# Kernel optimization log

Measured on AMD Instinct MI355X. Metric: run time of the kernel, lower is better.

The kernel has to match this reference:

```python
import jax, jax.numpy as jnp
import numpy as np

SEQ_LEN, INPUT_DIM, HIDDEN_DIM, OUTPUT_DIM = 512, 512, 1024, 512
BATCH = 64


def setup_inputs() -> dict:
    key = jax.random.key(0)
    k1, k2, k3, k4, k5 = jax.random.split(key, 5)
    fan_in_i2h = INPUT_DIM + HIDDEN_DIM
    s1 = 1.0 / np.sqrt(fan_in_i2h)
    s2 = 1.0 / np.sqrt(HIDDEN_DIM)
    return {
        "x": jax.random.normal(k1, (BATCH, SEQ_LEN, INPUT_DIM), dtype=jnp.float32),
        # i2h: Linear(input_dim+hidden_dim, 4*hidden_dim); stored as (in, out) for x @ W
        "W_i2h": jax.random.uniform(k2, (fan_in_i2h, 4 * HIDDEN_DIM), minval=-s1, maxval=s1, dtype=jnp.float32),
        "b_i2h": jax.random.uniform(k3, (4 * HIDDEN_DIM,), minval=-s1, maxval=s1, dtype=jnp.float32),
        # h2o: Linear(hidden_dim, output_dim)
        "W_h2o": jax.random.uniform(k4, (HIDDEN_DIM, OUTPUT_DIM), minval=-s2, maxval=s2, dtype=jnp.float32),
        "b_h2o": jax.random.uniform(k5, (OUTPUT_DIM,), minval=-s2, maxval=s2, dtype=jnp.float32),
    }


def reference(x, W_i2h, b_i2h, W_h2o, b_h2o):
    B = x.shape[0]
    H = W_h2o.shape[0]
    h0 = jnp.zeros((B, H), dtype=x.dtype)
    c0 = jnp.zeros((B, H), dtype=x.dtype)

    def step(carry, x_t):
        h_t, c_t = carry
        combined = jnp.concatenate([x_t, h_t], axis=1)  # [B, in+H]
        gates = combined @ W_i2h + b_i2h                # [B, 4H]
        i_t, f_t, g_t, o_t = jnp.split(gates, 4, axis=1)
        i_t = jax.nn.sigmoid(i_t)
        f_t = jax.nn.sigmoid(f_t)
        g_t = jnp.tanh(g_t)
        o_t = jax.nn.sigmoid(o_t)
        c_new = f_t * c_t + i_t * g_t
        h_new = o_t * jnp.tanh(c_new)
        return (h_new, c_new), None

    # scan over time: x [B, T, in] -> [T, B, in]
    (h_last, _), _ = jax.lax.scan(step, (h0, c0), jnp.swapaxes(x, 0, 1))
    # original returns only the last timestep's output projection
    return h_last @ W_h2o + b_h2o
```

## Files before the change

kernel.cpp:

```cpp
#include <hip/hip_runtime.h>
#include <hip/hip_bf16.h>
#include <stdint.h>


typedef __bf16 bf16x8 __attribute__((ext_vector_type(8)));
typedef float  f32x4  __attribute__((ext_vector_type(4)));
typedef unsigned long long u64;

#define NWG   256
#define NTHR  512

#define WS_FLAGS  0
#define WS_GO     2048
#define WS_HBUF   4096
#define HB_STRIDE 262144
#define HB_LO     131072
#define WS_HLAST  (WS_HBUF + 2*HB_STRIDE)

#define L_WHI   0
#define L_WLO   49152
#define L_EXCH  98304
#define L_EXCH2 102400
#define LDS_BYTES 106496

__device__ __forceinline__ float sigm(float x) {
    return __builtin_amdgcn_rcpf(1.0f + __expf(-x));
}
__device__ __forceinline__ float tanh_f(float x) {
    x = fminf(fmaxf(x, -20.0f), 20.0f);
    float e = __expf(-2.0f * x);
    return (1.0f - e) * __builtin_amdgcn_rcpf(1.0f + e);
}

__global__ void lstm_init(char* __restrict__ ws) {
    int id = blockIdx.x * 256 + threadIdx.x;
    for (int i = id; i < 66560; i += 256 * 256)
        __hip_atomic_store((unsigned*)ws + i, 0u,
                           __ATOMIC_RELAXED, __HIP_MEMORY_SCOPE_AGENT);
}

__global__ __launch_bounds__(NTHR) void lstm_main(
        const float* __restrict__ x, const float* __restrict__ Wi2h,
        const float* __restrict__ bi2h, const float* __restrict__ Wh2o,
        const float* __restrict__ bh2o, float* __restrict__ out,
        char* __restrict__ ws) {
    extern __shared__ char lds[];
    const int tid = threadIdx.x, wg = blockIdx.x;
    const int w = tid >> 6, lane = tid & 63, g = lane >> 4, nl = lane & 15;
    const int mt = w & 3, kh = w >> 2;

    for (int u = tid; u < 3072; u += NTHR) {
        int ak = u >> 4, cl = u & 15;
        int n = (cl >> 2) * 1024 + wg * 4 + (cl & 3);
        bf16x8 hi8, lo8;
#pragma unroll
        for (int j = 0; j < 8; ++j) {
            float v = Wi2h[(size_t)(ak * 8 + j) * 4096 + n];
            __bf16 h = (__bf16)v;
            hi8[j] = h;
            lo8[j] = (__bf16)(v - (float)h);
        }
        *(bf16x8*)(lds + L_WHI + (size_t)u * 16) = hi8;
        *(bf16x8*)(lds + L_WLO + (size_t)u * 16) = lo8;
    }
    const float bias_nl = bi2h[(nl >> 2) * 1024 + wg * 4 + (nl & 3)];
    __syncthreads();

    unsigned* flags = (unsigned*)(ws + WS_FLAGS);
    unsigned* go    = (unsigned*)(ws + WS_GO);
    float* exch  = (float*)(lds + L_EXCH);
    float* exch2 = (float*)(lds + L_EXCH2);
    float creg = 0.f;

#pragma unroll 1
    for (int t = 0; t < 512; ++t) {
        const char* hb_rd = ws + WS_HBUF + (size_t)(t & 1) * HB_STRIDE;
        char*       hb_wr = ws + WS_HBUF + (size_t)((t + 1) & 1) * HB_STRIDE;
        f32x4 acc0 = {0.f, 0.f, 0.f, 0.f}, acc1 = {0.f, 0.f, 0.f, 0.f};

        {
            const float* xb = x + ((size_t)(mt * 16 + nl) * 512 + t) * 512 + g * 8;
            const int s0 = kh * 8;
#pragma unroll
            for (int si = 0; si < 8; ++si) {
                const int s = s0 + si;
                float4 v0 = *(const float4*)(xb + s * 32);
                float4 v1 = *(const float4*)(xb + s * 32 + 4);
                float vv[8] = {v0.x, v0.y, v0.z, v0.w, v1.x, v1.y, v1.z, v1.w};
                bf16x8 ahi, alo;
#pragma unroll
                for (int j = 0; j < 8; ++j) {
                    __bf16 h = (__bf16)vv[j];
                    ahi[j] = h;
                    alo[j] = (__bf16)(vv[j] - (float)h);
                }
                const char* bp = lds + (size_t)(4 * s + g) * 256 + nl * 16;
                bf16x8 bhi = *(const bf16x8*)(bp + L_WHI);
                bf16x8 blo = *(const bf16x8*)(bp + L_WLO);
                if (s & 1) {
                    acc1 = __builtin_amdgcn_mfma_f32_16x16x32_bf16(ahi, bhi, acc1, 0, 0, 0);
                    acc1 = __builtin_amdgcn_mfma_f32_16x16x32_bf16(ahi, blo, acc1, 0, 0, 0);
                    acc1 = __builtin_amdgcn_mfma_f32_16x16x32_bf16(alo, bhi, acc1, 0, 0, 0);
                } else {
                    acc0 = __builtin_amdgcn_mfma_f32_16x16x32_bf16(ahi, bhi, acc0, 0, 0, 0);
                    acc0 = __builtin_amdgcn_mfma_f32_16x16x32_bf16(ahi, blo, acc0, 0, 0, 0);
                    acc0 = __builtin_amdgcn_mfma_f32_16x16x32_bf16(alo, bhi, acc0, 0, 0, 0);
                }
            }
        }

        if (tid == 0) {
            while (__hip_atomic_load(go, __ATOMIC_RELAXED,
                                     __HIP_MEMORY_SCOPE_AGENT) < (unsigned)t)
                __builtin_amdgcn_s_sleep(1);
        }
        __syncthreads();

        {
            const int s0 = 16 + kh * 16;
#pragma unroll 4
            for (int si = 0; si < 16; ++si) {
                const int s = s0 + si;
                size_t ha = ((size_t)(mt * 32 + (s - 16)) * 64 + lane) * 16;
                const char* bse = hb_rd + ha;
                u64 q0 = __hip_atomic_load((const u64*)(bse),
                           __ATOMIC_RELAXED, __HIP_MEMORY_SCOPE_AGENT);
                u64 q1 = __hip_atomic_load((const u64*)(bse + 8),
                           __ATOMIC_RELAXED, __HIP_MEMORY_SCOPE_AGENT);
                u64 q2 = __hip_atomic_load((const u64*)(bse + HB_LO),
                           __ATOMIC_RELAXED, __HIP_MEMORY_SCOPE_AGENT);
                u64 q3 = __hip_atomic_load((const u64*)(bse + HB_LO + 8),
                           __ATOMIC_RELAXED, __HIP_MEMORY_SCOPE_AGENT);
                union { u64 q[2]; bf16x8 v; } uh, ul;
                uh.q[0] = q0; uh.q[1] = q1;
                ul.q[0] = q2; ul.q[1] = q3;
                bf16x8 ahi = uh.v, alo = ul.v;
                const char* bp = lds + (size_t)(4 * s + g) * 256 + nl * 16;
                bf16x8 bhi = *(const bf16x8*)(bp + L_WHI);
                bf16x8 blo = *(const bf16x8*)(bp + L_WLO);
                if (s & 1) {
                    acc1 = __builtin_amdgcn_mfma_f32_16x16x32_bf16(ahi, bhi, acc1, 0, 0, 0);
                    acc1 = __builtin_amdgcn_mfma_f32_16x16x32_bf16(ahi, blo, acc1, 0, 0, 0);
                    acc1 = __builtin_amdgcn_mfma_f32_16x16x32_bf16(alo, bhi, acc1, 0, 0, 0);
                } else {
                    acc0 = __builtin_amdgcn_mfma_f32_16x16x32_bf16(ahi, bhi, acc0, 0, 0, 0);
                    acc0 = __builtin_amdgcn_mfma_f32_16x16x32_bf16(ahi, blo, acc0, 0, 0, 0);
                    acc0 = __builtin_amdgcn_mfma_f32_16x16x32_bf16(alo, bhi, acc0, 0, 0, 0);
                }
            }
        }

        if (kh == 1) {
#pragma unroll
            for (int j = 0; j < 4; ++j)
                exch[mt * 256 + (g * 4 + j) * 16 + nl] = acc0[j] + acc1[j];
        }
        __syncthreads();
        if (kh == 0) {
#pragma unroll
            for (int j = 0; j < 4; ++j) {
                float pre = acc0[j] + acc1[j] + exch[mt * 256 + (g * 4 + j) * 16 + nl]
                          + bias_nl;
                float act = ((nl >> 2) == 2) ? tanh_f(pre) : sigm(pre);
                exch2[mt * 256 + (g * 4 + j) * 16 + nl] = act;
            }
        }
        __syncthreads();
        if (tid < 256) {
            int mt2 = tid >> 6, r = (tid >> 2) & 15, hc = tid & 3;
            const float* a2 = exch2 + mt2 * 256 + r * 16;
            float iv = a2[hc], fv = a2[4 + hc], gv = a2[8 + hc], ov = a2[12 + hc];
            float cc = fv * creg + iv * gv;
            creg = cc;
            float hv = ov * tanh_f(cc);
            __bf16 hh = (__bf16)hv;
            __bf16 hl = (__bf16)(hv - (float)hh);
            int k = 512 + wg * 4 + hc;
            int hs = (k >> 5) - 16, kg = (k >> 3) & 3, j8 = k & 7;
            uint32_t ad = ((uint32_t)(mt2 * 32 + hs) * 64 + kg * 16 + r) * 16 + j8 * 2;
            __hip_atomic_store((unsigned short*)(hb_wr + ad),
                               __builtin_bit_cast(unsigned short, hh),
                               __ATOMIC_RELAXED, __HIP_MEMORY_SCOPE_AGENT);
            __hip_atomic_store((unsigned short*)(hb_wr + HB_LO + ad),
                               __builtin_bit_cast(unsigned short, hl),
                               __ATOMIC_RELAXED, __HIP_MEMORY_SCOPE_AGENT);
            if (t == 511)
                __hip_atomic_store((float*)(ws + WS_HLAST)
                                       + (mt2 * 16 + r) * 1024 + wg * 4 + hc, hv,
                                   __ATOMIC_RELAXED, __HIP_MEMORY_SCOPE_AGENT);
        }
        __syncthreads();
        if (tid == 0)
            __hip_atomic_store(&flags[wg], (unsigned)(t + 1),
                               __ATOMIC_RELAXED, __HIP_MEMORY_SCOPE_AGENT);
        if (wg == 0 && tid < 64) {
            unsigned tgt = (unsigned)(t + 1);
            for (;;) {
                unsigned f0 = __hip_atomic_load(flags + lane * 4 + 0, __ATOMIC_RELAXED, __HIP_MEMORY_SCOPE_AGENT);
                unsigned f1 = __hip_atomic_load(flags + lane * 4 + 1, __ATOMIC_RELAXED, __HIP_MEMORY_SCOPE_AGENT);
                unsigned f2 = __hip_atomic_load(flags + lane * 4 + 2, __ATOMIC_RELAXED, __HIP_MEMORY_SCOPE_AGENT);
                unsigned f3 = __hip_atomic_load(flags + lane * 4 + 3, __ATOMIC_RELAXED, __HIP_MEMORY_SCOPE_AGENT);
                unsigned mn = min(min(f0, f1), min(f2, f3));
                if (!__any(mn < tgt)) break;
                __builtin_amdgcn_s_sleep(1);
            }
            if (tid == 0)
                __hip_atomic_store(go, tgt, __ATOMIC_RELAXED, __HIP_MEMORY_SCOPE_AGENT);
        }
    }

    if (tid == 0) {
        while (__hip_atomic_load(go, __ATOMIC_RELAXED,
                                 __HIP_MEMORY_SCOPE_AGENT) < 512u)
            __builtin_amdgcn_s_sleep(1);
    }
    __syncthreads();
    __builtin_amdgcn_fence(__ATOMIC_ACQUIRE, "agent");

    const float* HL = (const float*)(ws + WS_HLAST);
    float* hl = (float*)lds;
    float* pp = (float*)(lds + 8192);
    int bb = wg & 63, q = wg >> 6;
    hl[tid]       = HL[bb * 1024 + tid];
    hl[tid + 512] = HL[bb * 1024 + 512 + tid];
    __syncthreads();
    int c = q * 128 + (tid & 127), kq = tid >> 7;
    const float* wc = Wh2o + c;
    float part = 0.f;
#pragma unroll 8
    for (int k = kq * 256; k < kq * 256 + 256; ++k)
        part += hl[k] * wc[(size_t)k * 512];
    pp[kq * 128 + (tid & 127)] = part;
    __syncthreads();
    if (tid < 128)
        out[bb * 512 + q * 128 + tid] =
            pp[tid] + pp[128 + tid] + pp[256 + tid] + pp[384 + tid] + bh2o[q * 128 + tid];
}

extern "C" void kernel_launch(void* const* d_in, const int* in_sizes, int n_in,
                              void* d_out, int out_size, void* d_ws, size_t ws_size,
                              hipStream_t stream) {
    const float* x    = (const float*)d_in[0];
    const float* Wi2h = (const float*)d_in[1];
    const float* bi2h = (const float*)d_in[2];
    const float* Wh2o = (const float*)d_in[3];
    const float* bh2o = (const float*)d_in[4];
    float* out = (float*)d_out;
    char* ws = (char*)d_ws;

    hipFuncSetAttribute(reinterpret_cast<const void*>(lstm_main),
                        hipFuncAttributeMaxDynamicSharedMemorySize, LDS_BYTES);

    lstm_init<<<256, 256, 0, stream>>>(ws);

    void* args[] = {(void*)&x, (void*)&Wi2h, (void*)&bi2h, (void*)&Wh2o,
                    (void*)&bh2o, (void*)&out, (void*)&ws};
    hipLaunchCooperativeKernel(reinterpret_cast<void*>(lstm_main),
                               dim3(NWG), dim3(NTHR), args, LDS_BYTES, stream);
}
```

Measured before the change: 5.396 ms.

## Replace shared go flag with per-workgroup mailboxes and spin without sleep

The grid barrier's single shared 'go' word, which all 256 workgroups polled, is replaced by per-workgroup mailbox words padded to 64 bytes. Workgroup 0's first wave writes the release value into each mailbox once all flags are observed. The s_sleep calls are removed from both spin loops, and the flag gather uses 64-bit loads. This is meant to cut barrier latency and contention on one cache line across 512 timesteps, at the cost of heavier spinning traffic. The hidden-state loop unroll also goes from 4 to 8.

```diff
diff --git a/kernel.cpp b/kernel.cpp
--- a/kernel.cpp
+++ b/kernel.cpp
@@ -11,8 +11,8 @@
 #define NTHR  512
 
 #define WS_FLAGS  0
-#define WS_GO     2048
-#define WS_HBUF   4096
+#define WS_GOMB   1024
+#define WS_HBUF   17408
 #define HB_STRIDE 262144
 #define HB_LO     131072
 #define WS_HLAST  (WS_HBUF + 2*HB_STRIDE)
@@ -34,7 +34,7 @@
 
 __global__ void lstm_init(char* __restrict__ ws) {
     int id = blockIdx.x * 256 + threadIdx.x;
-    for (int i = id; i < 66560; i += 256 * 256)
+    for (int i = id; i < 69888; i += 256 * 256)
         __hip_atomic_store((unsigned*)ws + i, 0u,
                            __ATOMIC_RELAXED, __HIP_MEMORY_SCOPE_AGENT);
 }
@@ -67,7 +67,7 @@
     __syncthreads();
 
     unsigned* flags = (unsigned*)(ws + WS_FLAGS);
-    unsigned* go    = (unsigned*)(ws + WS_GO);
+    unsigned* my_mb = (unsigned*)(ws + WS_GOMB) + wg * 16;
     float* exch  = (float*)(lds + L_EXCH);
     float* exch2 = (float*)(lds + L_EXCH2);
     float creg = 0.f;
@@ -110,15 +110,14 @@
         }
 
         if (tid == 0) {
-            while (__hip_atomic_load(go, __ATOMIC_RELAXED,
-                                     __HIP_MEMORY_SCOPE_AGENT) < (unsigned)t)
-                __builtin_amdgcn_s_sleep(1);
+            while (__hip_atomic_load(my_mb, __ATOMIC_RELAXED,
+                                     __HIP_MEMORY_SCOPE_AGENT) < (unsigned)t) {}
         }
         __syncthreads();
 
         {
             const int s0 = 16 + kh * 16;
-#pragma unroll 4
+#pragma unroll 8
             for (int si = 0; si < 16; ++si) {
                 const int s = s0 + si;
                 size_t ha = ((size_t)(mt * 32 + (s - 16)) * 64 + lane) * 16;
@@ -193,26 +192,29 @@
         if (tid == 0)
             __hip_atomic_store(&flags[wg], (unsigned)(t + 1),
                                __ATOMIC_RELAXED, __HIP_MEMORY_SCOPE_AGENT);
-        if (wg == 0 && tid < 64) {
+        if (wg == 0 && w == 0) {
             unsigned tgt = (unsigned)(t + 1);
+            const u64* f64 = (const u64*)flags;
             for (;;) {
-                unsigned f0 = __hip_atomic_load(flags + lane * 4 + 0, __ATOMIC_RELAXED, __HIP_MEMORY_SCOPE_AGENT);
-                unsigned f1 = __hip_atomic_load(flags + lane * 4 + 1, __ATOMIC_RELAXED, __HIP_MEMORY_SCOPE_AGENT);
-                unsigned f2 = __hip_atomic_load(flags + lane * 4 + 2, __ATOMIC_RELAXED, __HIP_MEMORY_SCOPE_AGENT);
-                unsigned f3 = __hip_atomic_load(flags + lane * 4 + 3, __ATOMIC_RELAXED, __HIP_MEMORY_SCOPE_AGENT);
-                unsigned mn = min(min(f0, f1), min(f2, f3));
-                if (!__any(mn < tgt)) break;
-                __builtin_amdgcn_s_sleep(1);
-            }
-            if (tid == 0)
-                __hip_atomic_store(go, tgt, __ATOMIC_RELAXED, __HIP_MEMORY_SCOPE_AGENT);
+                u64 a = __hip_atomic_load(f64 + 2 * lane,
+                          __ATOMIC_RELAXED, __HIP_MEMORY_SCOPE_AGENT);
+                u64 b = __hip_atomic_load(f64 + 2 * lane + 1,
+                          __ATOMIC_RELAXED, __HIP_MEMORY_SCOPE_AGENT);
+                unsigned m0 = min(min((unsigned)a, (unsigned)(a >> 32)),
+                                  min((unsigned)b, (unsigned)(b >> 32)));
+                if (__all(m0 >= tgt)) break;
+            }
+            unsigned* mb = (unsigned*)(ws + WS_GOMB);
+#pragma unroll
+            for (int q = 0; q < 4; ++q)
+                __hip_atomic_store(mb + (q * 64 + lane) * 16, tgt,
+                                   __ATOMIC_RELAXED, __HIP_MEMORY_SCOPE_AGENT);
         }
     }
 
     if (tid == 0) {
-        while (__hip_atomic_load(go, __ATOMIC_RELAXED,
-                                 __HIP_MEMORY_SCOPE_AGENT) < 512u)
-            __builtin_amdgcn_s_sleep(1);
+        while (__hip_atomic_load(my_mb, __ATOMIC_RELAXED,
+                                 __HIP_MEMORY_SCOPE_AGENT) < 512u) {}
     }
     __syncthreads();
     __builtin_amdgcn_fence(__ATOMIC_ACQUIRE, "agent");
```

New measurement: 5.293 ms. About the same (-1.9%).
